# Optimization experiments

Hardware: AMD Instinct MI355X
Metric: run time of the kernel (lower is better)

Reference implementation:

```python
import jax, jax.numpy as jnp
import numpy as np


def setup_inputs() -> dict:
    key = jax.random.key(0)
    kx, kd = jax.random.split(key)
    B, T, D = 16, 1024, 512
    x = jax.random.normal(kx, (B, T, D), dtype=jnp.float32)
    durations = jax.random.randint(kd, (B, T), 0, 8, dtype=jnp.int64)
    return {"x": x, "durations": durations, "max_len": 4096}


def reference(x, durations, max_len):
    # x: [B,T,D], durations: [B,T] int, max_len: static int
    B, T, D = x.shape
    dur = jnp.maximum(durations.astype(jnp.int32), 0)          # clamp(min=0)
    csum = jnp.cumsum(dur, axis=1)                              # [B,T] inclusive cumsum
    total = csum[:, -1]                                         # [B] total frames per row
    pos = jnp.arange(max_len, dtype=jnp.int32)                  # [L] output frame indices
    # source token for output frame j: first t with csum[t] > j (== repeat_interleave)
    src = jax.vmap(lambda c: jnp.searchsorted(c, pos, side='right'))(csum)  # [B,L]
    src = jnp.minimum(src, T - 1)                               # clamp for out-of-range frames
    out = jnp.take_along_axis(x, src[..., None], axis=1)        # [B,L,D] single parallel gather
    mask = pos[None, :] < total[:, None]                        # [B,L] valid frames
    return jnp.where(mask[..., None], out, jnp.zeros((), x.dtype))
```

## Files before the change

kernel.cpp:

```cpp
#include <hip/hip_runtime.h>


#define BB 16
#define TT 1024
#define DD 512
#define MAXLEN 4096

__global__ __launch_bounds__(256) void build_src_kernel(
    const int* __restrict__ dur, int* __restrict__ srcTab) {
  const int b = blockIdx.x;
  const int tid = threadIdx.x;

  __shared__ int lds[256];
  __shared__ int s_total;

  const int t0 = tid * 4;
  const int* dp = dur + b * TT + t0;
  int d0 = max(dp[0], 0);
  int d1 = max(dp[1], 0);
  int d2 = max(dp[2], 0);
  int d3 = max(dp[3], 0);
  const int s1 = d0 + d1;
  const int s2 = s1 + d2;
  const int s3 = s2 + d3;

  lds[tid] = s3;
  __syncthreads();

  int val = s3;
  for (int off = 1; off < 256; off <<= 1) {
    int other = (tid >= off) ? lds[tid - off] : 0;
    __syncthreads();
    val += other;
    lds[tid] = val;
    __syncthreads();
  }
  const int incl = val;
  const int excl = incl - s3;

  if (tid == 255) s_total = incl;
  __syncthreads();
  const int total = s_total;

  int c[4] = {excl + d0, excl + s1, excl + s2, excl + s3};
  int dd4[4] = {d0, d1, d2, d3};
  int* st = srcTab + b * MAXLEN;
#pragma unroll
  for (int j = 0; j < 4; ++j) {
    const int end = c[j];
    for (int p = end - dd4[j]; p < end; ++p) st[p] = t0 + j;
  }
  for (int p = total + tid; p < MAXLEN; p += 256) st[p] = -1;
}

__global__ __launch_bounds__(256) void gather_kernel(
    const float4* __restrict__ x, const int* __restrict__ srcTab,
    float4* __restrict__ out) {
  const int wave = (int)((blockIdx.x * 256u + threadIdx.x) >> 6);
  const int lane = threadIdx.x & 63;
  const int row = wave;
  const int b = row >> 12;
  const int src = srcTab[row];

  float4* op = out + (size_t)row * (DD / 4);
  if (src < 0) {
    const float4 z = {0.f, 0.f, 0.f, 0.f};
    op[lane] = z;
    op[lane + 64] = z;
  } else {
    const float4* ip = x + ((size_t)b * TT + (size_t)src) * (DD / 4);
    op[lane] = ip[lane];
    op[lane + 64] = ip[lane + 64];
  }
}

extern "C" void kernel_launch(void* const* d_in, const int* in_sizes, int n_in,
                              void* d_out, int out_size, void* d_ws,
                              size_t ws_size, hipStream_t stream) {
  const float* x = (const float*)d_in[0];
  const int* dur = (const int*)d_in[1];
  int* srcTab = (int*)d_ws;

  build_src_kernel<<<BB, 256, 0, stream>>>(dur, srcTab);

  const int rows = BB * MAXLEN;
  gather_kernel<<<rows / 4, 256, 0, stream>>>((const float4*)x, srcTab,
                                              (float4*)d_out);
}
```

Measured before the change: 161.3 us.

## Use wave-shuffle scan, nontemporal stores, and XCD-aware block remap in gather

The prefix-sum kernel now uses 1024 threads, one token per thread, with wave shuffle scans in place of the LDS Hillis-Steele loop and its many barriers. The gather kernel writes output with nontemporal stores so the large streaming output does not pollute cache. It also remaps block IDs so consecutive logical blocks, each covering rows that share source rows, land on the same XCD. The risk is that the nontemporal hint or the remap could hurt L2 reuse of x rows that are repeated across frames.

```diff
diff --git a/kernel.cpp b/kernel.cpp
--- a/kernel.cpp
+++ b/kernel.cpp
@@ -6,71 +6,64 @@
 #define DD 512
 #define MAXLEN 4096
 
-__global__ __launch_bounds__(256) void build_src_kernel(
+typedef float f32x4 __attribute__((ext_vector_type(4)));
+
+__global__ __launch_bounds__(1024) void build_src_kernel(
     const int* __restrict__ dur, int* __restrict__ srcTab) {
   const int b = blockIdx.x;
-  const int tid = threadIdx.x;
+  const int t = threadIdx.x;
+  const int lane = t & 63;
+  const int wid = t >> 6;
 
-  __shared__ int lds[256];
-  __shared__ int s_total;
+  __shared__ int wsum[16];
 
-  const int t0 = tid * 4;
-  const int* dp = dur + b * TT + t0;
-  int d0 = max(dp[0], 0);
-  int d1 = max(dp[1], 0);
-  int d2 = max(dp[2], 0);
-  int d3 = max(dp[3], 0);
-  const int s1 = d0 + d1;
-  const int s2 = s1 + d2;
-  const int s3 = s2 + d3;
+  int d = dur[b * TT + t];
+  d = d > 0 ? d : 0;
 
-  lds[tid] = s3;
+  int v = d;
+#pragma unroll
+  for (int off = 1; off < 64; off <<= 1) {
+    int o = __shfl_up(v, off, 64);
+    if (lane >= off) v += o;
+  }
+  if (lane == 63) wsum[wid] = v;
   __syncthreads();
 
-  int val = s3;
-  for (int off = 1; off < 256; off <<= 1) {
-    int other = (tid >= off) ? lds[tid - off] : 0;
-    __syncthreads();
-    val += other;
-    lds[tid] = val;
-    __syncthreads();
+  int base = 0, total = 0;
+#pragma unroll
+  for (int w = 0; w < 16; ++w) {
+    const int s = wsum[w];
+    total += s;
+    if (w < wid) base += s;
   }
-  const int incl = val;
-  const int excl = incl - s3;
+  const int incl = base + v;
 
-  if (tid == 255) s_total = incl;
-  __syncthreads();
-  const int total = s_total;
-
-  int c[4] = {excl + d0, excl + s1, excl + s2, excl + s3};
-  int dd4[4] = {d0, d1, d2, d3};
   int* st = srcTab + b * MAXLEN;
-#pragma unroll
-  for (int j = 0; j < 4; ++j) {
-    const int end = c[j];
-    for (int p = end - dd4[j]; p < end; ++p) st[p] = t0 + j;
-  }
-  for (int p = total + tid; p < MAXLEN; p += 256) st[p] = -1;
+  for (int p = incl - d; p < incl; ++p) st[p] = t;
+  for (int p = total + t; p < MAXLEN; p += 1024) st[p] = -1;
 }
 
 __global__ __launch_bounds__(256) void gather_kernel(
-    const float4* __restrict__ x, const int* __restrict__ srcTab,
-    float4* __restrict__ out) {
-  const int wave = (int)((blockIdx.x * 256u + threadIdx.x) >> 6);
-  const int lane = threadIdx.x & 63;
-  const int row = wave;
+    const f32x4* __restrict__ x, const int* __restrict__ srcTab,
+    f32x4* __restrict__ out) {
+  const int bid = (int)blockIdx.x;
+  const int lb = (bid & 7) * (16384 >> 3) + (bid >> 3);
+  const int row = (lb << 2) | ((int)threadIdx.x >> 6);
+  const int lane = (int)threadIdx.x & 63;
   const int b = row >> 12;
   const int src = srcTab[row];
 
-  float4* op = out + (size_t)row * (DD / 4);
+  f32x4* op = out + (size_t)row * (DD / 4);
   if (src < 0) {
-    const float4 z = {0.f, 0.f, 0.f, 0.f};
-    op[lane] = z;
-    op[lane + 64] = z;
+    const f32x4 z = {0.f, 0.f, 0.f, 0.f};
+    __builtin_nontemporal_store(z, op + lane);
+    __builtin_nontemporal_store(z, op + lane + 64);
   } else {
-    const float4* ip = x + ((size_t)b * TT + (size_t)src) * (DD / 4);
-    op[lane] = ip[lane];
-    op[lane + 64] = ip[lane + 64];
+    const f32x4* ip = x + ((size_t)b * TT + (size_t)src) * (DD / 4);
+    const f32x4 a = ip[lane];
+    const f32x4 c = ip[lane + 64];
+    __builtin_nontemporal_store(a, op + lane);
+    __builtin_nontemporal_store(c, op + lane + 64);
   }
 }
 
@@ -81,9 +74,9 @@
   const int* dur = (const int*)d_in[1];
   int* srcTab = (int*)d_ws;
 
-  build_src_kernel<<<BB, 256, 0, stream>>>(dur, srcTab);
+  build_src_kernel<<<BB, 1024, 0, stream>>>(dur, srcTab);
 
   const int rows = BB * MAXLEN;
-  gather_kernel<<<rows / 4, 256, 0, stream>>>((const float4*)x, srcTab,
-                                              (float4*)d_out);
+  gather_kernel<<<rows / 4, 256, 0, stream>>>((const f32x4*)x, srcTab,
+                                              (f32x4*)d_out);
 }
```

Result: slower. 170.1 us (+5.5%).
